# Kernel tuning notes

Hardware: AMD Instinct MI355X
Metric: run time of the kernel (lower is better)

## Reference

```python
import jax, jax.numpy as jnp
import numpy as np

N_NODES = 100000
N_EDGES = 3200000
NFEAT = 512
NCLASS = 40
DIMS = [NFEAT, 256, 128, 64, NCLASS]


def _glorot(key, fan_in, fan_out):
    lim = 1.0 / np.sqrt(fan_out)
    return jax.random.uniform(key, (fan_in, fan_out), jnp.float32, -lim, lim)


def setup_inputs() -> dict:
    key = jax.random.key(0)
    ks = jax.random.split(key, 16)
    inp = {
        'x': jax.random.normal(ks[0], (N_NODES, NFEAT), jnp.float32),
        'edge_src': jax.random.randint(ks[1], (N_EDGES,), 0, N_NODES, jnp.int32),
        'edge_dst': jax.random.randint(ks[2], (N_EDGES,), 0, N_NODES, jnp.int32),
        'edge_weight': jax.random.uniform(ks[3], (N_EDGES,), jnp.float32),
    }
    for i in range(4):
        inp[f'W{i+1}'] = _glorot(ks[4 + 2 * i], DIMS[i], DIMS[i + 1])
        lim = 1.0 / np.sqrt(DIMS[i + 1])
        inp[f'b{i+1}'] = jax.random.uniform(ks[5 + 2 * i], (DIMS[i + 1],), jnp.float32, -lim, lim)
    return inp


def _gc_layer(h, W, b, src, dst, ew):
    # support = h @ W ; out = spmm(adj, support) + b
    support = h @ W                                   # [N, d_out]
    msgs = support[src] * ew[:, None]                 # gather + scale per edge
    agg = jax.ops.segment_sum(msgs, dst, num_segments=N_NODES)
    return agg + b


def reference(x, edge_src, edge_dst, edge_weight, W1, b1, W2, b2, W3, b3, W4, b4):
    h = x
    for W, b in ((W1, b1), (W2, b2), (W3, b3), (W4, b4)):
        h = jax.nn.relu(_gc_layer(h, W, b, edge_src, edge_dst, edge_weight))
    return jax.nn.log_softmax(h, axis=1)
```

## Files before the change

kernel.cpp:

```cpp
#include <hip/hip_runtime.h>
#include <hip/hip_bf16.h>
#include <math.h>
#include <stdint.h>


#define WAVE 64
#define NBK 512
#define CHA 8192
typedef __attribute__((ext_vector_type(8))) short short8;
typedef __attribute__((ext_vector_type(8))) unsigned short ushort8;
typedef __attribute__((ext_vector_type(4))) unsigned int uintx4;
typedef __attribute__((ext_vector_type(4))) float floatx4;
typedef __attribute__((ext_vector_type(2))) float floatx2;

__device__ __forceinline__ void async_copy16(const void* g, void* l) {
    __builtin_amdgcn_global_load_lds(
        (const __attribute__((address_space(1))) void*)g,
        (__attribute__((address_space(3))) void*)l, 16, 0, 0);
}
__device__ __forceinline__ float bf2f(unsigned short u) {
    union { unsigned int i; float f; } x; x.i = ((unsigned int)u) << 16; return x.f;
}


__global__ __launch_bounds__(256) void convert_x_kernel(const float* __restrict__ in,
                                                        __hip_bfloat16* __restrict__ out,
                                                        long n4) {
    long i = ((long)blockIdx.x * 256 + threadIdx.x);
    if (i >= n4) return;
    const float4 v = *(const float4*)(in + i * 4);
    __hip_bfloat16* o = out + i * 4;
    o[0] = __float2bfloat16(v.x); o[1] = __float2bfloat16(v.y);
    o[2] = __float2bfloat16(v.z); o[3] = __float2bfloat16(v.w);
}

__global__ __launch_bounds__(256) void prep_weights_kernel(
        const float* __restrict__ W1, const float* __restrict__ W2,
        const float* __restrict__ W3, const float* __restrict__ W4,
        const float* __restrict__ b4,
        __hip_bfloat16* __restrict__ Wt1, __hip_bfloat16* __restrict__ Wt2,
        __hip_bfloat16* __restrict__ Wt3, __hip_bfloat16* __restrict__ Wt4,
        float* __restrict__ b4p) {
    int idx = blockIdx.x * 256 + threadIdx.x;
    if (idx < 131072) {
        int n = idx >> 9, k = idx & 511;
        Wt1[idx] = __float2bfloat16(W1[(size_t)k * 256 + n]);
    } else if (idx < 131072 + 32768) {
        int l = idx - 131072;
        int n = l >> 8, k = l & 255;
        Wt2[l] = __float2bfloat16(W2[(size_t)k * 128 + n]);
    } else if (idx < 131072 + 32768 + 8192) {
        int l = idx - 131072 - 32768;
        int n = l >> 7, k = l & 127;
        Wt3[l] = __float2bfloat16(W3[(size_t)k * 64 + n]);
    } else if (idx < 131072 + 32768 + 8192 + 4096) {
        int l = idx - 131072 - 32768 - 8192;
        int n = l >> 6, k = l & 63;
        float v = (n < 40) ? W4[(size_t)k * 40 + n] : 0.f;
        Wt4[l] = __float2bfloat16(v);
    } else if (idx < 131072 + 32768 + 8192 + 4096 + 64) {
        int l = idx - 131072 - 32768 - 8192 - 4096;
        b4p[l] = (l < 40) ? b4[l] : 0.f;
    }
}


__global__ __launch_bounds__(256) void bucket_hist(const int* __restrict__ dst,
                                                   int nE, int* __restrict__ bhist) {
    __shared__ int h[NBK];
    const int t = threadIdx.x;
    const long e0 = (long)blockIdx.x * CHA;
    const int cnt = (int)((nE - e0 < CHA) ? (nE - e0) : CHA);
    for (int i = t; i < NBK; i += 256) h[i] = 0;
    __syncthreads();
    for (int i = t; i < cnt; i += 256)
        atomicAdd(&h[dst[e0 + i] >> 8], 1);
    __syncthreads();
    for (int i = t; i < NBK; i += 256)
        if (h[i]) atomicAdd(&bhist[i], h[i]);
}

__global__ __launch_bounds__(512) void bucket_scan(const int* __restrict__ bhist,
                                                   int* __restrict__ bbase,
                                                   int* __restrict__ gcur) {
    __shared__ int sm[NBK];
    const int t = threadIdx.x;
    int x = bhist[t];
    sm[t] = x;
    __syncthreads();
    for (int off = 1; off < NBK; off <<= 1) {
        int add = (t >= off) ? sm[t - off] : 0;
        __syncthreads();
        if (t >= off) sm[t] += add;
        __syncthreads();
    }
    int excl = sm[t] - x;
    bbase[t] = excl;
    gcur[t] = excl;
    if (t == NBK - 1) bbase[NBK] = sm[t];
}

__global__ __launch_bounds__(256) void scatter_phaseA(const int* __restrict__ src,
                                                      const int* __restrict__ dst,
                                                      const float* __restrict__ ew,
                                                      int nE,
                                                      int* __restrict__ gcur,
                                                      uint2* __restrict__ E2) {
    __shared__ int hist[NBK];
    __shared__ int cur[NBK];
    const int t = threadIdx.x;
    const long e0 = (long)blockIdx.x * CHA;
    const int cnt = (int)((nE - e0 < CHA) ? (nE - e0) : CHA);

    for (int i = t; i < NBK; i += 256) hist[i] = 0;
    __syncthreads();
    for (int i = t; i < cnt; i += 256)
        atomicAdd(&hist[dst[e0 + i] >> 8], 1);
    __syncthreads();
    for (int i = t; i < NBK; i += 256) {
        int h = hist[i];
        cur[i] = h ? atomicAdd(&gcur[i], h) : 0;
    }
    __syncthreads();
    for (int i = t; i < cnt; i += 256) {
        int d = dst[e0 + i];
        unsigned int w15 = (unsigned int)(ew[e0 + i] * 32767.f + 0.5f);
        if (w15 > 32767u) w15 = 32767u;
        int pos = atomicAdd(&cur[d >> 8], 1);
        E2[pos] = make_uint2(((unsigned int)src[e0 + i] << 15) | w15,
                             (unsigned int)d);
    }
}

__global__ __launch_bounds__(256) void scatter_phaseB2(const uint2* __restrict__ E2,
                                                       const int* __restrict__ bbase,
                                                       int n_nodes, int nE,
                                                       int* __restrict__ row_ptr,
                                                       unsigned int* __restrict__ edge_pk) {
    __shared__ int cnt[256];
    __shared__ int pfx[256];
    __shared__ int cur[256];
    const int b = blockIdx.x;
    const int t = threadIdx.x;
    const int s = bbase[b];
    const int e = bbase[b + 1];

    cnt[t] = 0;
    __syncthreads();
    for (int i = s + t; i < e; i += 256)
        atomicAdd(&cnt[E2[i].y & 255], 1);
    __syncthreads();
    pfx[t] = cnt[t];
    __syncthreads();
    for (int off = 1; off < 256; off <<= 1) {
        int add = (t >= off) ? pfx[t - off] : 0;
        __syncthreads();
        if (t >= off) pfx[t] += add;
        __syncthreads();
    }
    const int excl = pfx[t] - cnt[t];
    const int node = b * 256 + t;
    if (node < n_nodes) row_ptr[node] = s + excl;
    if (b == 0 && t == 0) row_ptr[n_nodes] = nE;
    cur[t] = s + excl;
    __syncthreads();
    for (int i = s + t; i < e; i += 256) {
        uint2 ed = E2[i];
        int p = atomicAdd(&cur[ed.y & 255], 1);
        edge_pk[p] = ed.x;
    }
}


template <int OUTM>
__global__ __launch_bounds__(256) void gemm_bf16(const __hip_bfloat16* __restrict__ A,
                                                 const __hip_bfloat16* __restrict__ Wt,
                                                 void* __restrict__ C,
                                                 int M, int K, int Npitch) {
    __shared__ __align__(16) __hip_bfloat16 sA[128 * 64];
    __shared__ __align__(16) __hip_bfloat16 sB[64 * 64];
    const int t = threadIdx.x;
    const int lane = t & 63;
    const int w = t >> 6;
    const int wy = w >> 1, wx = w & 1;
    const int quad = lane >> 4;
    const int l16 = lane & 15;
    const int row0 = blockIdx.y * 128;
    const int col0 = blockIdx.x * 64;

    floatx4 acc[4][2];
#pragma unroll
    for (int mt = 0; mt < 4; mt++)
#pragma unroll
        for (int nt = 0; nt < 2; nt++) acc[mt][nt] = 0;

    const int arow = t >> 3;
    const int koff = (t & 7) * 8;

    for (int k0 = 0; k0 < K; k0 += 64) {
#pragma unroll
        for (int r = 0; r < 4; r++) {
            int gm = row0 + r * 32 + arow;
            int gmc = (gm < M) ? gm : 0;
            async_copy16(A + (size_t)gmc * K + k0 + koff,
                         (char*)sA + r * 4096 + t * 16);
        }
#pragma unroll
        for (int r = 0; r < 2; r++) {
            int n = r * 32 + arow;
            async_copy16(Wt + (size_t)(col0 + n) * K + k0 + koff,
                         (char*)sB + r * 4096 + t * 16);
        }
        __syncthreads();

        short8 af[4][2], bfr[2][2];
#pragma unroll
        for (int mt = 0; mt < 4; mt++)
#pragma unroll
            for (int kk = 0; kk < 2; kk++)
                af[mt][kk] = *(const short8*)((const char*)sA +
                             (wy * 64 + mt * 16 + l16) * 128 + kk * 64 + quad * 16);
#pragma unroll
        for (int nt = 0; nt < 2; nt++)
#pragma unroll
            for (int kk = 0; kk < 2; kk++)
                bfr[nt][kk] = *(const short8*)((const char*)sB +
                              (wx * 32 + nt * 16 + l16) * 128 + kk * 64 + quad * 16);
#pragma unroll
        for (int kk = 0; kk < 2; kk++)
#pragma unroll
            for (int mt = 0; mt < 4; mt++)
#pragma unroll
                for (int nt = 0; nt < 2; nt++)
                    acc[mt][nt] = __builtin_amdgcn_mfma_f32_16x16x32_bf16(
                        af[mt][kk], bfr[nt][kk], acc[mt][nt], 0, 0, 0);
        __syncthreads();
    }

#pragma unroll
    for (int mt = 0; mt < 4; mt++) {
#pragma unroll
        for (int nt = 0; nt < 2; nt++) {
            int gn = col0 + wx * 32 + nt * 16 + l16;
            int gmb = row0 + wy * 64 + mt * 16 + quad * 4;
#pragma unroll
            for (int r = 0; r < 4; r++) {
                int gm = gmb + r;
                if (gm < M) {
                    if (OUTM == 0) {
                        ((__hip_bfloat16*)C)[(size_t)gm * Npitch + gn] =
                            __float2bfloat16(acc[mt][nt][r]);
                    } else {
                        float v = acc[mt][nt][r];
                        int p = __builtin_amdgcn_cvt_pk_fp8_f32(v, v, 0, false);
                        ((unsigned char*)C)[(size_t)gm * Npitch + gn] =
                            (unsigned char)(p & 0xff);
                    }
                }
            }
        }
    }
}


template <int D, int U>
__global__ __launch_bounds__(256) void spmm_fp8(const int* __restrict__ row_ptr,
                                                const unsigned int* __restrict__ edge_pk,
                                                const unsigned char* __restrict__ sup8,
                                                const float* __restrict__ bias,
                                                __hip_bfloat16* __restrict__ out,
                                                int n_nodes) {
    constexpr int G = D / 16;
    constexpr int NG = 64 / G;
    constexpr int CH = NG * U;
    int node = blockIdx.x * (256 / WAVE) + (threadIdx.x >> 6);
    if (node >= n_nodes) return;
    node = __builtin_amdgcn_readfirstlane(node);
    const int lane = threadIdx.x & 63;
    const int g = lane / G;
    const int t = lane & (G - 1);
    int e = row_ptr[node];
    const int end = row_ptr[node + 1];
    const unsigned char* sup = sup8 + t * 16;

    float acc[16];
#pragma unroll
    for (int i = 0; i < 16; i++) acc[i] = 0.f;

    while (e < end) {
        const int base = e + g * U;
        unsigned int pk[U];
#pragma unroll
        for (int u = 0; u < U; u++) {
            int idx = base + u;
            if (idx > end - 1) idx = end - 1;
            pk[u] = edge_pk[idx];
        }
        uintx4 v[U];
#pragma unroll
        for (int u = 0; u < U; u++)
            v[u] = *(const uintx4*)(sup + (size_t)(pk[u] >> 15) * D);
#pragma unroll
        for (int u = 0; u < U; u++) {
            float wq = (float)(pk[u] & 0x7fffu) * (1.f / 32767.f);
            float wt = (base + u < end) ? wq : 0.f;
#pragma unroll
            for (int d = 0; d < 4; d++) {
                floatx2 lo = __builtin_amdgcn_cvt_pk_f32_fp8(v[u][d], false);
                floatx2 hi = __builtin_amdgcn_cvt_pk_f32_fp8(v[u][d], true);
                acc[d * 4 + 0] += lo[0] * wt;
                acc[d * 4 + 1] += lo[1] * wt;
                acc[d * 4 + 2] += hi[0] * wt;
                acc[d * 4 + 3] += hi[1] * wt;
            }
        }
        e += CH;
    }

#pragma unroll
    for (int off = G; off < 64; off <<= 1)
#pragma unroll
        for (int i = 0; i < 16; i++) acc[i] += __shfl_xor(acc[i], off);

    if (lane < G) {
        ushort8 o0, o1;
#pragma unroll
        for (int i = 0; i < 8; i++) {
            float r0 = acc[i] + bias[t * 16 + i];
            float r1 = acc[8 + i] + bias[t * 16 + 8 + i];
            r0 = r0 > 0.f ? r0 : 0.f;
            r1 = r1 > 0.f ? r1 : 0.f;
            __hip_bfloat16 b0 = __float2bfloat16(r0);
            __hip_bfloat16 b1 = __float2bfloat16(r1);
            o0[i] = *(unsigned short*)&b0;
            o1[i] = *(unsigned short*)&b1;
        }
        union { ushort8 s; uintx4 u; } c0, c1; c0.s = o0; c1.s = o1;
        unsigned short* op = (unsigned short*)out + (size_t)node * D + t * 16;
        __builtin_nontemporal_store(c0.u, (uintx4*)op);
        __builtin_nontemporal_store(c1.u, (uintx4*)(op + 8));
    }
}


template <int D, int G, int U, bool FINAL, typename OT>
__global__ __launch_bounds__(256) void spmm_bias_relu(const int* __restrict__ row_ptr,
                                                      const unsigned int* __restrict__ edge_pk,
                                                      const __hip_bfloat16* __restrict__ support,
                                                      const float* __restrict__ bias,
                                                      OT* __restrict__ out,
                                                      int n_nodes) {
    constexpr int NG = 64 / G;
    constexpr int CH = NG * U;
    int node = blockIdx.x * (256 / WAVE) + (threadIdx.x >> 6);
    if (node >= n_nodes) return;
    node = __builtin_amdgcn_readfirstlane(node);
    const int lane = threadIdx.x & 63;
    const int g = lane / G;
    const int t = lane & (G - 1);
    int e = row_ptr[node];
    const int end = row_ptr[node + 1];
    const unsigned short* sup = (const unsigned short*)support + t * 8;

    float acc[8];
#pragma unroll
    for (int i = 0; i < 8; i++) acc[i] = 0.f;

    while (e < end) {
        const int base = e + g * U;
        unsigned int pk[U];
#pragma unroll
        for (int u = 0; u < U; u++) {
            int idx = base + u;
            if (idx > end - 1) idx = end - 1;
            pk[u] = edge_pk[idx];
        }
        ushort8 v[U];
#pragma unroll
        for (int u = 0; u < U; u++)
            v[u] = *(const ushort8*)(sup + (size_t)(pk[u] >> 15) * D);
#pragma unroll
        for (int u = 0; u < U; u++) {
            float wq = (float)(pk[u] & 0x7fffu) * (1.f / 32767.f);
            float wt = (base + u < end) ? wq : 0.f;
#pragma unroll
            for (int i = 0; i < 8; i++) acc[i] += bf2f(v[u][i]) * wt;
        }
        e += CH;
    }

#pragma unroll
    for (int off = G; off < 64; off <<= 1)
#pragma unroll
        for (int i = 0; i < 8; i++) acc[i] += __shfl_xor(acc[i], off);

    if (!FINAL) {
        ushort8 o;
#pragma unroll
        for (int i = 0; i < 8; i++) {
            float r = acc[i] + bias[t * 8 + i];
            r = r > 0.f ? r : 0.f;
            __hip_bfloat16 b = __float2bfloat16(r);
            o[i] = *(unsigned short*)&b;
        }
        if (lane < G) {
            union { ushort8 s; uintx4 u; } cvt; cvt.s = o;
            __builtin_nontemporal_store(cvt.u,
                (uintx4*)((unsigned short*)out + (size_t)node * D + t * 8));
        }
    } else {
        float r[8];
#pragma unroll
        for (int i = 0; i < 8; i++) {
            float x = acc[i] + bias[t * 8 + i];
            r[i] = x > 0.f ? x : 0.f;
        }
        float m = -INFINITY;
#pragma unroll
        for (int i = 0; i < 8; i++)
            if (t * 8 + i < 40) m = fmaxf(m, r[i]);
#pragma unroll
        for (int off = 1; off < G; off <<= 1) m = fmaxf(m, __shfl_xor(m, off));
        float s = 0.f;
#pragma unroll
        for (int i = 0; i < 8; i++)
            if (t * 8 + i < 40) s += __expf(r[i] - m);
#pragma unroll
        for (int off = 1; off < G; off <<= 1) s += __shfl_xor(s, off);
        const float lse = __logf(s);
        if (lane < 5) {
            float* op = (float*)out + (size_t)node * 40 + lane * 8;
#pragma unroll
            for (int i = 0; i < 8; i++) op[i] = r[i] - m - lse;
        }
    }
}


extern "C" void kernel_launch(void* const* d_in, const int* in_sizes, int n_in,
                              void* d_out, int out_size, void* d_ws, size_t ws_size,
                              hipStream_t stream) {
    const float* x    = (const float*)d_in[0];
    const int*   esrc = (const int*)d_in[1];
    const int*   edst = (const int*)d_in[2];
    const float* ew   = (const float*)d_in[3];
    const float* Wm[4] = {(const float*)d_in[4], (const float*)d_in[6],
                          (const float*)d_in[8], (const float*)d_in[10]};
    const float* bm[4] = {(const float*)d_in[5], (const float*)d_in[7],
                          (const float*)d_in[9], (const float*)d_in[11]};
    const int NFEAT = 512;
    const int n_nodes = in_sizes[0] / NFEAT;
    const int n_edges = in_sizes[1];
    float* out = (float*)d_out;

    char* wsp = (char*)d_ws;
    size_t off = 0;
    auto alloc = [&](size_t bytes) -> void* {
        void* p = wsp + off;
        off += (bytes + 255) & ~(size_t)255;
        return p;
    };
    __hip_bfloat16* Xb = (__hip_bfloat16*)alloc((size_t)n_nodes * 512 * sizeof(__hip_bfloat16));
    __hip_bfloat16* Sb = (__hip_bfloat16*)alloc((size_t)n_nodes * 256 * sizeof(__hip_bfloat16));
    __hip_bfloat16* Hb = (__hip_bfloat16*)alloc((size_t)n_nodes * 256 * sizeof(__hip_bfloat16));
    __hip_bfloat16* Wt1 = (__hip_bfloat16*)alloc(256 * 512 * sizeof(__hip_bfloat16));
    __hip_bfloat16* Wt2 = (__hip_bfloat16*)alloc(128 * 256 * sizeof(__hip_bfloat16));
    __hip_bfloat16* Wt3 = (__hip_bfloat16*)alloc(64 * 128 * sizeof(__hip_bfloat16));
    __hip_bfloat16* Wt4 = (__hip_bfloat16*)alloc(64 * 64 * sizeof(__hip_bfloat16));
    float* b4p     = (float*)alloc(64 * sizeof(float));
    int*   row_ptr = (int*)alloc(((size_t)n_nodes + 1) * sizeof(int));
    int*   bhist   = (int*)alloc(NBK * sizeof(int));
    int*   bbase   = (int*)alloc((NBK + 1) * sizeof(int));
    int*   gcur    = (int*)alloc(NBK * sizeof(int));
    unsigned int* edge_pk = (unsigned int*)alloc((size_t)n_edges * sizeof(unsigned int));
    uint2* E2 = (uint2*)Hb;
    unsigned char* Sb8 = (unsigned char*)Sb;
    (void)ws_size;

    long n4 = (long)n_nodes * 512 / 4;
    convert_x_kernel<<<(int)((n4 + 255) / 256), 256, 0, stream>>>(x, Xb, n4);
    prep_weights_kernel<<<(131072 + 32768 + 8192 + 4096 + 64 + 255) / 256, 256, 0, stream>>>(
        Wm[0], Wm[1], Wm[2], Wm[3], bm[3], Wt1, Wt2, Wt3, Wt4, b4p);

    hipMemsetAsync(bhist, 0, NBK * sizeof(int), stream);
    int hblocks = (n_edges + CHA - 1) / CHA;
    bucket_hist<<<hblocks, 256, 0, stream>>>(edst, n_edges, bhist);
    bucket_scan<<<1, NBK, 0, stream>>>(bhist, bbase, gcur);
    scatter_phaseA<<<hblocks, 256, 0, stream>>>(esrc, edst, ew, n_edges, gcur, E2);
    scatter_phaseB2<<<NBK, 256, 0, stream>>>(E2, bbase, n_nodes, n_edges,
                                             row_ptr, edge_pk);

    int spmm_blocks = (n_nodes + 3) / 4;
    dim3 g1(256 / 64, (n_nodes + 127) / 128);
    dim3 g2(128 / 64, (n_nodes + 127) / 128);
    dim3 g3(64 / 64, (n_nodes + 127) / 128);

    gemm_bf16<1><<<g1, 256, 0, stream>>>(Xb, Wt1, Sb8, n_nodes, 512, 256);
    spmm_fp8<256, 4><<<spmm_blocks, 256, 0, stream>>>(
        row_ptr, edge_pk, Sb8, bm[0], Hb, n_nodes);
    gemm_bf16<1><<<g2, 256, 0, stream>>>(Hb, Wt2, Sb8, n_nodes, 256, 128);
    spmm_fp8<128, 2><<<spmm_blocks, 256, 0, stream>>>(
        row_ptr, edge_pk, Sb8, bm[1], Hb, n_nodes);
    gemm_bf16<1><<<g3, 256, 0, stream>>>(Hb, Wt3, Sb8, n_nodes, 128, 64);
    spmm_fp8<64, 1><<<spmm_blocks, 256, 0, stream>>>(
        row_ptr, edge_pk, Sb8, bm[2], Hb, n_nodes);
    gemm_bf16<0><<<g3, 256, 0, stream>>>(Hb, Wt4, Sb, n_nodes, 64, 64);
    spmm_bias_relu<64, 8, 2, true, float><<<spmm_blocks, 256, 0, stream>>>(
        row_ptr, edge_pk, Sb, b4p, out, n_nodes);
}
```

Baseline: 837.9 us.

## Fuse fp32-to-bf16 input conversion into a wider 128-column GEMM and use fp8 in the final layer

Removes the separate pass that converts x to bf16 and instead converts fp32 tiles to bf16 while loading them into LDS inside a new 128x128-tile GEMM. Layers 1 and 2 use this wider tile for more reuse. The last layer now writes fp8 support and reuses the fp8 SpMM kernel with a fused log-softmax epilogue, halving gather bytes. The costs are synchronous fp32 loads in layer 1 instead of async copies, plus extra quantization error in the final layer.

Measured after the change: 825.5 us. Within noise of the previous version (-1.5%).

```diff
diff --git a/kernel.cpp b/kernel.cpp
--- a/kernel.cpp
+++ b/kernel.cpp
@@ -17,21 +17,6 @@
     __builtin_amdgcn_global_load_lds(
         (const __attribute__((address_space(1))) void*)g,
         (__attribute__((address_space(3))) void*)l, 16, 0, 0);
-}
-__device__ __forceinline__ float bf2f(unsigned short u) {
-    union { unsigned int i; float f; } x; x.i = ((unsigned int)u) << 16; return x.f;
-}
-
-
-__global__ __launch_bounds__(256) void convert_x_kernel(const float* __restrict__ in,
-                                                        __hip_bfloat16* __restrict__ out,
-                                                        long n4) {
-    long i = ((long)blockIdx.x * 256 + threadIdx.x);
-    if (i >= n4) return;
-    const float4 v = *(const float4*)(in + i * 4);
-    __hip_bfloat16* o = out + i * 4;
-    o[0] = __float2bfloat16(v.x); o[1] = __float2bfloat16(v.y);
-    o[2] = __float2bfloat16(v.z); o[3] = __float2bfloat16(v.w);
 }
 
 __global__ __launch_bounds__(256) void prep_weights_kernel(
@@ -172,6 +157,121 @@
 }
 
 
+template <int AFP32, int OUTM>
+__global__ __launch_bounds__(256) void gemm128(const void* __restrict__ Av,
+                                               const __hip_bfloat16* __restrict__ Wt,
+                                               void* __restrict__ C,
+                                               int M, int K, int Npitch) {
+    __shared__ __align__(16) __hip_bfloat16 sA[128 * 64];
+    __shared__ __align__(16) __hip_bfloat16 sB[128 * 64];
+    const int t = threadIdx.x;
+    const int lane = t & 63;
+    const int w = t >> 6;
+    const int wy = w >> 1, wx = w & 1;
+    const int quad = lane >> 4;
+    const int l16 = lane & 15;
+    const int row0 = blockIdx.y * 128;
+    const int col0 = blockIdx.x * 128;
+
+    floatx4 acc[4][4];
+#pragma unroll
+    for (int mt = 0; mt < 4; mt++)
+#pragma unroll
+        for (int nt = 0; nt < 4; nt++) acc[mt][nt] = 0;
+
+    const int arow = t >> 3;
+    const int koff = (t & 7) * 8;
+
+    for (int k0 = 0; k0 < K; k0 += 64) {
+        if (AFP32) {
+            float4 fa[4][2];
+#pragma unroll
+            for (int r = 0; r < 4; r++) {
+                int gm = row0 + r * 32 + arow;
+                int gmc = (gm < M) ? gm : 0;
+                const float* ap = (const float*)Av + (size_t)gmc * K + k0 + koff;
+                fa[r][0] = *(const float4*)ap;
+                fa[r][1] = *(const float4*)(ap + 4);
+            }
+#pragma unroll
+            for (int r = 0; r < 4; r++) {
+                ushort8 pk;
+#pragma unroll
+                for (int i = 0; i < 4; i++) {
+                    __hip_bfloat16 b0 = __float2bfloat16(((const float*)&fa[r][0])[i]);
+                    __hip_bfloat16 b1 = __float2bfloat16(((const float*)&fa[r][1])[i]);
+                    pk[i] = *(unsigned short*)&b0;
+                    pk[4 + i] = *(unsigned short*)&b1;
+                }
+                *(ushort8*)((char*)sA + r * 4096 + t * 16) = pk;
+            }
+        } else {
+#pragma unroll
+            for (int r = 0; r < 4; r++) {
+                int gm = row0 + r * 32 + arow;
+                int gmc = (gm < M) ? gm : 0;
+                async_copy16((const __hip_bfloat16*)Av + (size_t)gmc * K + k0 + koff,
+                             (char*)sA + r * 4096 + t * 16);
+            }
+        }
+#pragma unroll
+        for (int r = 0; r < 4; r++) {
+            int n = r * 32 + arow;
+            async_copy16(Wt + (size_t)(col0 + n) * K + k0 + koff,
+                         (char*)sB + r * 4096 + t * 16);
+        }
+        __syncthreads();
+
+        short8 af[4][2], bfr[4][2];
+#pragma unroll
+        for (int mt = 0; mt < 4; mt++)
+#pragma unroll
+            for (int kk = 0; kk < 2; kk++)
+                af[mt][kk] = *(const short8*)((const char*)sA +
+                             (wy * 64 + mt * 16 + l16) * 128 + kk * 64 + quad * 16);
+#pragma unroll
+        for (int nt = 0; nt < 4; nt++)
+#pragma unroll
+            for (int kk = 0; kk < 2; kk++)
+                bfr[nt][kk] = *(const short8*)((const char*)sB +
+                              (wx * 64 + nt * 16 + l16) * 128 + kk * 64 + quad * 16);
+#pragma unroll
+        for (int kk = 0; kk < 2; kk++)
+#pragma unroll
+            for (int mt = 0; mt < 4; mt++)
+#pragma unroll
+                for (int nt = 0; nt < 4; nt++)
+                    acc[mt][nt] = __builtin_amdgcn_mfma_f32_16x16x32_bf16(
+                        af[mt][kk], bfr[nt][kk], acc[mt][nt], 0, 0, 0);
+        __syncthreads();
+    }
+
+#pragma unroll
+    for (int mt = 0; mt < 4; mt++) {
+#pragma unroll
+        for (int nt = 0; nt < 4; nt++) {
+            int gn = col0 + wx * 64 + nt * 16 + l16;
+            int gmb = row0 + wy * 64 + mt * 16 + quad * 4;
+#pragma unroll
+            for (int r = 0; r < 4; r++) {
+                int gm = gmb + r;
+                if (gm < M) {
+                    if (OUTM == 0) {
+                        ((__hip_bfloat16*)C)[(size_t)gm * Npitch + gn] =
+                            __float2bfloat16(acc[mt][nt][r]);
+                    } else {
+                        float v = acc[mt][nt][r];
+                        int p = __builtin_amdgcn_cvt_pk_fp8_f32(v, v, 0, false);
+                        ((unsigned char*)C)[(size_t)gm * Npitch + gn] =
+                            (unsigned char)(p & 0xff);
+                    }
+                }
+            }
+        }
+    }
+}
+
+
 template <int OUTM>
 __global__ __launch_bounds__(256) void gemm_bf16(const __hip_bfloat16* __restrict__ A,
                                                  const __hip_bfloat16* __restrict__ Wt,
@@ -263,12 +363,12 @@
 }
 
 
-template <int D, int U>
+template <int D, int U, bool FINAL>
 __global__ __launch_bounds__(256) void spmm_fp8(const int* __restrict__ row_ptr,
                                                 const unsigned int* __restrict__ edge_pk,
                                                 const unsigned char* __restrict__ sup8,
                                                 const float* __restrict__ bias,
-                                                __hip_bfloat16* __restrict__ out,
+                                                void* __restrict__ out,
                                                 int n_nodes) {
     constexpr int G = D / 16;
     constexpr int NG = 64 / G;
@@ -322,116 +422,52 @@
 #pragma unroll
         for (int i = 0; i < 16; i++) acc[i] += __shfl_xor(acc[i], off);
 
-    if (lane < G) {
-        ushort8 o0, o1;
-#pragma unroll
-        for (int i = 0; i < 8; i++) {
-            float r0 = acc[i] + bias[t * 16 + i];
-            float r1 = acc[8 + i] + bias[t * 16 + 8 + i];
-            r0 = r0 > 0.f ? r0 : 0.f;
-            r1 = r1 > 0.f ? r1 : 0.f;
-            __hip_bfloat16 b0 = __float2bfloat16(r0);
-            __hip_bfloat16 b1 = __float2bfloat16(r1);
-            o0[i] = *(unsigned short*)&b0;
-            o1[i] = *(unsigned short*)&b1;
-        }
-        union { ushort8 s; uintx4 u; } c0, c1; c0.s = o0; c1.s = o1;
-        unsigned short* op = (unsigned short*)out + (size_t)node * D + t * 16;
-        __builtin_nontemporal_store(c0.u, (uintx4*)op);
-        __builtin_nontemporal_store(c1.u, (uintx4*)(op + 8));
-    }
-}
-
-
-template <int D, int G, int U, bool FINAL, typename OT>
-__global__ __launch_bounds__(256) void spmm_bias_relu(const int* __restrict__ row_ptr,
-                                                      const unsigned int* __restrict__ edge_pk,
-                                                      const __hip_bfloat16* __restrict__ support,
-                                                      const float* __restrict__ bias,
-                                                      OT* __restrict__ out,
-                                                      int n_nodes) {
-    constexpr int NG = 64 / G;
-    constexpr int CH = NG * U;
-    int node = blockIdx.x * (256 / WAVE) + (threadIdx.x >> 6);
-    if (node >= n_nodes) return;
-    node = __builtin_amdgcn_readfirstlane(node);
-    const int lane = threadIdx.x & 63;
-    const int g = lane / G;
-    const int t = lane & (G - 1);
-    int e = row_ptr[node];
-    const int end = row_ptr[node + 1];
-    const unsigned short* sup = (const unsigned short*)support + t * 8;
-
-    float acc[8];
-#pragma unroll
-    for (int i = 0; i < 8; i++) acc[i] = 0.f;
-
-    while (e < end) {
-        const int base = e + g * U;
-        unsigned int pk[U];
-#pragma unroll
-        for (int u = 0; u < U; u++) {
-            int idx = base + u;
-            if (idx > end - 1) idx = end - 1;
-            pk[u] = edge_pk[idx];
-        }
-        ushort8 v[U];
-#pragma unroll
-        for (int u = 0; u < U; u++)
-            v[u] = *(const ushort8*)(sup + (size_t)(pk[u] >> 15) * D);
-#pragma unroll
-        for (int u = 0; u < U; u++) {
-            float wq = (float)(pk[u] & 0x7fffu) * (1.f / 32767.f);
-            float wt = (base + u < end) ? wq : 0.f;
-#pragma unroll
-            for (int i = 0; i < 8; i++) acc[i] += bf2f(v[u][i]) * wt;
-        }
-        e += CH;
-    }
-
-#pragma unroll
-    for (int off = G; off < 64; off <<= 1)
-#pragma unroll
-        for (int i = 0; i < 8; i++) acc[i] += __shfl_xor(acc[i], off);
-
     if (!FINAL) {
-        ushort8 o;
-#pragma unroll
-        for (int i = 0; i < 8; i++) {
-            float r = acc[i] + bias[t * 8 + i];
-            r = r > 0.f ? r : 0.f;
-            __hip_bfloat16 b = __float2bfloat16(r);
-            o[i] = *(unsigned short*)&b;
-        }
         if (lane < G) {
-            union { ushort8 s; uintx4 u; } cvt; cvt.s = o;
-            __builtin_nontemporal_store(cvt.u,
-                (uintx4*)((unsigned short*)out + (size_t)node * D + t * 8));
+            ushort8 o0, o1;
+#pragma unroll
+            for (int i = 0; i < 8; i++) {
+                float r0 = acc[i] + bias[t * 16 + i];
+                float r1 = acc[8 + i] + bias[t * 16 + 8 + i];
+                r0 = r0 > 0.f ? r0 : 0.f;
+                r1 = r1 > 0.f ? r1 : 0.f;
+                __hip_bfloat16 b0 = __float2bfloat16(r0);
+                __hip_bfloat16 b1 = __float2bfloat16(r1);
+                o0[i] = *(unsigned short*)&b0;
+                o1[i] = *(unsigned short*)&b1;
+            }
+            union { ushort8 s; uintx4 u; } c0, c1; c0.s = o0; c1.s = o1;
+            unsigned short* op = (unsigned short*)out + (size_t)node * D + t * 16;
+            __builtin_nontemporal_store(c0.u, (uintx4*)op);
+            __builtin_nontemporal_store(c1.u, (uintx4*)(op + 8));
         }
     } else {
-        float r[8];
-#pragma unroll
-        for (int i = 0; i < 8; i++) {
-            float x = acc[i] + bias[t * 8 + i];
+        float r[16];
+#pragma unroll
+        for (int i = 0; i < 16; i++) {
+            float x = acc[i] + bias[t * 16 + i];
             r[i] = x > 0.f ? x : 0.f;
         }
         float m = -INFINITY;
 #pragma unroll
-        for (int i = 0; i < 8; i++)
-            if (t * 8 + i < 40) m = fmaxf(m, r[i]);
+        for (int i = 0; i < 16; i++)
+            if (t * 16 + i < 40) m = fmaxf(m, r[i]);
 #pragma unroll
         for (int off = 1; off < G; off <<= 1) m = fmaxf(m, __shfl_xor(m, off));
         float s = 0.f;
 #pragma unroll
-        for (int i = 0; i < 8; i++)
-            if (t * 8 + i < 40) s += __expf(r[i] - m);
+        for (int i = 0; i < 16; i++)
+            if (t * 16 + i < 40) s += __expf(r[i] - m);
 #pragma unroll
         for (int off = 1; off < G; off <<= 1) s += __shfl_xor(s, off);
         const float lse = __logf(s);
-        if (lane < 5) {
-            float* op = (float*)out + (size_t)node * 40 + lane * 8;
-#pragma unroll
-            for (int i = 0; i < 8; i++) op[i] = r[i] - m - lse;
+        if (lane < G) {
+            float* op = (float*)out + (size_t)node * 40;
+#pragma unroll
+            for (int i = 0; i < 16; i++) {
+                int c = t * 16 + i;
+                if (c < 40) op[c] = r[i] - m - lse;
+            }
         }
     }
 }
@@ -460,7 +496,6 @@
         off += (bytes + 255) & ~(size_t)255;
         return p;
     };
-    __hip_bfloat16* Xb = (__hip_bfloat16*)alloc((size_t)n_nodes * 512 * sizeof(__hip_bfloat16));
     __hip_bfloat16* Sb = (__hip_bfloat16*)alloc((size_t)n_nodes * 256 * sizeof(__hip_bfloat16));
     __hip_bfloat16* Hb = (__hip_bfloat16*)alloc((size_t)n_nodes * 256 * sizeof(__hip_bfloat16));
     __hip_bfloat16* Wt1 = (__hip_bfloat16*)alloc(256 * 512 * sizeof(__hip_bfloat16));
@@ -477,8 +512,6 @@
     unsigned char* Sb8 = (unsigned char*)Sb;
     (void)ws_size;
 
-    long n4 = (long)n_nodes * 512 / 4;
-    convert_x_kernel<<<(int)((n4 + 255) / 256), 256, 0, stream>>>(x, Xb, n4);
     prep_weights_kernel<<<(131072 + 32768 + 8192 + 4096 + 64 + 255) / 256, 256, 0, stream>>>(
         Wm[0], Wm[1], Wm[2], Wm[3], bm[3], Wt1, Wt2, Wt3, Wt4, b4p);
 
@@ -491,20 +524,20 @@
                                              row_ptr, edge_pk);
 
     int spmm_blocks = (n_nodes + 3) / 4;
-    dim3 g1(256 / 64, (n_nodes + 127) / 128);
-    dim3 g2(128 / 64, (n_nodes + 127) / 128);
+    dim3 gg1(256 / 128, (n_nodes + 127) / 128);
+    dim3 gg2(128 / 128, (n_nodes + 127) / 128);
     dim3 g3(64 / 64, (n_nodes + 127) / 128);
 
-    gemm_bf16<1><<<g1, 256, 0, stream>>>(Xb, Wt1, Sb8, n_nodes, 512, 256);
-    spmm_fp8<256, 4><<<spmm_blocks, 256, 0, stream>>>(
+    gemm128<1, 1><<<gg1, 256, 0, stream>>>(x, Wt1, Sb8, n_nodes, 512, 256);
+    spmm_fp8<256, 4, false><<<spmm_blocks, 256, 0, stream>>>(
         row_ptr, edge_pk, Sb8, bm[0], Hb, n_nodes);
-    gemm_bf16<1><<<g2, 256, 0, stream>>>(Hb, Wt2, Sb8, n_nodes, 256, 128);
-    spmm_fp8<128, 2><<<spmm_blocks, 256, 0, stream>>>(
+    gemm128<0, 1><<<gg2, 256, 0, stream>>>(Hb, Wt2, Sb8, n_nodes, 256, 128);
+    spmm_fp8<128, 2, false><<<spmm_blocks, 256, 0, stream>>>(
         row_ptr, edge_pk, Sb8, bm[1], Hb, n_nodes);
     gemm_bf16<1><<<g3, 256, 0, stream>>>(Hb, Wt3, Sb8, n_nodes, 128, 64);
-    spmm_fp8<64, 1><<<spmm_blocks, 256, 0, stream>>>(
+    spmm_fp8<64, 1, false><<<spmm_blocks, 256, 0, stream>>>(
         row_ptr, edge_pk, Sb8, bm[2], Hb, n_nodes);
-    gemm_bf16<0><<<g3, 256, 0, stream>>>(Hb, Wt4, Sb, n_nodes, 64, 64);
-    spmm_bias_relu<64, 8, 2, true, float><<<spmm_blocks, 256, 0, stream>>>(
-        row_ptr, edge_pk, Sb, b4p, out, n_nodes);
-}
+    gemm_bf16<1><<<g3, 256, 0, stream>>>(Hb, Wt4, Sb8, n_nodes, 64, 64);
+    spmm_fp8<64, 1, true><<<spmm_blocks, 256, 0, stream>>>(
+        row_ptr, edge_pk, Sb8, b4p, out, n_nodes);
+}
```
